# Kernel tuning notes

Measured on AMD Instinct MI355X. Metric: run time of the kernel, lower is better.

The kernel has to match this reference:

```python
import jax, jax.numpy as jnp
import numpy as np

NEG_SLOPE = 0.2


def _seg_sum(x, ids, n):
    return jax.ops.segment_sum(x, ids, num_segments=n)


def _seg_softmax(score, ids, n):
    # numerically stable segment softmax over segments `ids`
    m = jax.ops.segment_max(score, ids, num_segments=n)
    ex = jnp.exp(score - m[ids])
    denom = _seg_sum(ex, ids, n)
    return ex / denom[ids]


def _seg_mean(x, ids, n):
    s = _seg_sum(x, ids, n)
    cnt = _seg_sum(jnp.ones(ids.shape[0], x.dtype), ids, n)
    return jnp.where(cnt[:, None] > 0, s / jnp.maximum(cnt, 1.0)[:, None], 0.0)


def _dphgnn(X, V, E, S, Wx, bx, Wv, bv, a, Wt, bt, num_nodes, num_edges):
    X_init = X @ Wx + bx                         # [N, H]
    X_feat = X @ Wv + bv                         # [N, H]
    score_node = X_feat @ a                      # [N]
    score = jax.nn.leaky_relu(score_node[V], NEG_SLOPE)   # [nnz]
    w = _seg_softmax(score, E, num_edges)        # [nnz]
    Xev = X_feat[V] * w[:, None]                 # [nnz, H] gather + weight
    Y_v2e = jax.nn.elu(_seg_sum(Xev, E, num_edges))       # [M, H]
    e_msg = jnp.concatenate([Y_v2e, S], axis=1)  # [M, H+star]
    Y = e_msg @ Wt + bt                          # [M, H]
    Xn = _seg_mean(Y[E], V, num_nodes)           # [N, H]
    Xn = jax.nn.elu(Xn)                          # is_last=False, dropout=eval
    return Xn + X_init


def _hyperconv(X, V, E, Wf, bf, num_nodes, num_edges):
    Xn = X @ Wf + bf
    Y = _seg_mean(Xn[V], E, num_edges)           # [M, O]
    ones = jnp.ones(V.shape[0], jnp.float32)
    D_v = _seg_sum(ones, V, num_nodes)           # node degrees
    cnt_e = _seg_sum(ones, E, num_edges)
    # torch scatter_reduce(mean, include_self=True): zero init counts as one element
    De = _seg_sum(D_v[V], E, num_edges) / (cnt_e + 1.0)
    De_inv = jnp.where(De > 0, De ** -0.5, 1.0)
    Y = De_inv[:, None] * Y
    Xo = _seg_sum(Y[E], V, num_nodes)
    Dv_inv = jnp.where(D_v > 0, D_v ** -0.5, 0.0)
    return Dv_inv[:, None] * Xo                  # is_last=True: no relu/dropout


def setup_inputs() -> dict:
    key = jax.random.key(0)
    ks = jax.random.split(key, 24)
    N, M, NNZ = 50000, 20000, 400000
    IN, H, OUT, STAR = 128, 256, 128, 64

    def lin(k, i, o):
        s = 1.0 / np.sqrt(i)
        k1, k2 = jax.random.split(k)
        return (jax.random.uniform(k1, (i, o), jnp.float32, -s, s),
                jax.random.uniform(k2, (o,), jnp.float32, -s, s))

    X = jax.random.normal(ks[0], (N, IN), jnp.float32)
    V = jax.random.randint(ks[1], (NNZ,), 0, N).at[-1].set(N - 1)
    E = jax.random.randint(ks[2], (NNZ,), 0, M).at[-1].set(M - 1)
    S = jax.random.normal(ks[3], (M, STAR), jnp.float32)

    Wx0, bx0 = lin(ks[4], IN, H)
    Wv0, bv0 = lin(ks[5], IN, H)
    a0 = jax.random.uniform(ks[6], (H,), jnp.float32, -1/np.sqrt(H), 1/np.sqrt(H))
    Wt0, bt0 = lin(ks[7], H + STAR, H)
    Wx1, bx1 = lin(ks[8], H, H)
    Wv1, bv1 = lin(ks[9], H, H)
    a1 = jax.random.uniform(ks[10], (H,), jnp.float32, -1/np.sqrt(H), 1/np.sqrt(H))
    Wt1, bt1 = lin(ks[11], H + STAR, H)
    Wf, bf = lin(ks[12], H, OUT)

    return dict(X=X, V=V, E=E, S=S,
                Wx0=Wx0, bx0=bx0, Wv0=Wv0, bv0=bv0, a0=a0, Wt0=Wt0, bt0=bt0,
                Wx1=Wx1, bx1=bx1, Wv1=Wv1, bv1=bv1, a1=a1, Wt1=Wt1, bt1=bt1,
                Wf=Wf, bf=bf)


def reference(X, V, E, S, Wx0, bx0, Wv0, bv0, a0, Wt0, bt0,
              Wx1, bx1, Wv1, bv1, a1, Wt1, bt1, Wf, bf):
    N = X.shape[0]
    M = S.shape[0]
    h = _dphgnn(X, V, E, S, Wx0, bx0, Wv0, bv0, a0, Wt0, bt0, N, M)
    h = _dphgnn(h, V, E, S, Wx1, bx1, Wv1, bv1, a1, Wt1, bt1, N, M)
    out = _hyperconv(h, V, E, Wf, bf, N, M)
    return out
```

## Files before the change

### kernel.cpp

```cpp
#include <hip/hip_runtime.h>

typedef unsigned short u16;
typedef __attribute__((ext_vector_type(4))) u16 u16x4;
typedef __attribute__((ext_vector_type(8))) u16 u16x8;
typedef __attribute__((ext_vector_type(8))) _Float16 f16x8;
typedef __attribute__((ext_vector_type(4))) float f32x4;

__device__ __forceinline__ u16 f2h(float x) {
    _Float16 h = (_Float16)x;
    return __builtin_bit_cast(u16, h);
}
__device__ __forceinline__ float h2f(u16 u) {
    return (float)__builtin_bit_cast(_Float16, u);
}

__device__ __forceinline__ void gl_lds16(const void* g, void* l) {
    __builtin_amdgcn_global_load_lds(
        (const __attribute__((address_space(1))) void*)g,
        (__attribute__((address_space(3))) void*)l, 16, 0, 0);
}

__global__ __launch_bounds__(256) void gemm_mfma_kernel(
    const u16* __restrict__ A, int lda,
    const u16* __restrict__ B, int ldb,
    const float* __restrict__ biasF, const float* __restrict__ biasB,
    u16* __restrict__ CbA, u16* __restrict__ CbB,
    const float* __restrict__ avec, float* __restrict__ scoreOut,
    int M, int Nc, int ncSplit, int K, int nrb, int ncb)
{
    int g = blockIdx.x;
    int xcd = g & 7;
    int slot = g >> 3;
    int rbi = slot / ncb;
    int cb = slot - rbi * ncb;
    int rb = xcd + 8 * rbi;
    if (rb >= nrb) return;

    __shared__ __align__(16) u16 lds[12288];
    u16* sA0 = lds;
    u16* sA1 = lds + 4096;
    u16* sB0 = lds + 8192;
    u16* sB1 = lds + 10240;

    int tid = threadIdx.x;
    int wave = tid >> 6, lane = tid & 63;
    int row0 = rb * 128, col0 = cb * 64;

    long gA[2];
    int sOffA[2];
#pragma unroll
    for (int r = 0; r < 2; ++r) {
        int trow = r * 64 + wave * 16 + (lane >> 2);
        int chunk = (lane & 3) ^ ((trow >> 2) & 3);
        int arow = min(row0 + trow, M - 1);
        gA[r] = (long)arow * lda + chunk * 8;
        sOffA[r] = (r * 64 + wave * 16) * 32;
    }
    int trowB = wave * 16 + (lane >> 2);
    int chunkB = (lane & 3) ^ ((trowB >> 2) & 3);
    long gB = (long)(col0 + trowB) * ldb + chunkB * 8;
    int sOffB = (wave * 16) * 32;

    int m16 = lane & 15, quad = lane >> 4;
    int offA[4], offB[2];
#pragma unroll
    for (int i = 0; i < 4; ++i) {
        int ra = (wave & 1) * 64 + i * 16 + m16;
        offA[i] = ra * 32 + ((quad ^ ((ra >> 2) & 3)) * 8);
    }
#pragma unroll
    for (int j = 0; j < 2; ++j) {
        int rbx = (wave >> 1) * 32 + j * 16 + m16;
        offB[j] = rbx * 32 + ((quad ^ ((rbx >> 2) & 3)) * 8);
    }

    f32x4 acc[4][2];
#pragma unroll
    for (int i = 0; i < 4; ++i)
#pragma unroll
        for (int j = 0; j < 2; ++j) {
            f32x4 z = {0.f, 0.f, 0.f, 0.f};
            acc[i][j] = z;
        }

    int nkb = K >> 6;
    for (int kb = 0; kb < nkb; ++kb) {
#pragma unroll
        for (int r = 0; r < 2; ++r) {
            gl_lds16(A + gA[r], sA0 + sOffA[r]);
            gl_lds16(A + gA[r] + 32, sA1 + sOffA[r]);
        }
        gl_lds16(B + gB, sB0 + sOffB);
        gl_lds16(B + gB + 32, sB1 + sOffB);
        __syncthreads();
        {
            f16x8 av[4], bv[2];
#pragma unroll
            for (int i = 0; i < 4; ++i) av[i] = *(const f16x8*)(sA0 + offA[i]);
#pragma unroll
            for (int j = 0; j < 2; ++j) bv[j] = *(const f16x8*)(sB0 + offB[j]);
#pragma unroll
            for (int i = 0; i < 4; ++i)
#pragma unroll
                for (int j = 0; j < 2; ++j)
                    acc[i][j] = __builtin_amdgcn_mfma_f32_16x16x32_f16(av[i], bv[j], acc[i][j], 0, 0, 0);
        }
        {
            f16x8 av[4], bv[2];
#pragma unroll
            for (int i = 0; i < 4; ++i) av[i] = *(const f16x8*)(sA1 + offA[i]);
#pragma unroll
            for (int j = 0; j < 2; ++j) bv[j] = *(const f16x8*)(sB1 + offB[j]);
#pragma unroll
            for (int i = 0; i < 4; ++i)
#pragma unroll
                for (int j = 0; j < 2; ++j)
                    acc[i][j] = __builtin_amdgcn_mfma_f32_16x16x32_f16(av[i], bv[j], acc[i][j], 0, 0, 0);
        }
        __syncthreads();
#pragma unroll
        for (int r = 0; r < 2; ++r) gA[r] += 64;
        gB += 64;
    }

    int rbase = (wave & 1) * 64, cbase = (wave >> 1) * 32;
    float bj[2];
#pragma unroll
    for (int j = 0; j < 2; ++j) {
        int col = col0 + cbase + j * 16 + m16;
        bj[j] = (col >= ncSplit) ? biasB[col - ncSplit] : biasF[col];
    }
    u16* wlds = lds + wave * 2560;
    __syncthreads();
#pragma unroll
    for (int j = 0; j < 2; ++j)
#pragma unroll
        for (int i = 0; i < 4; ++i)
#pragma unroll
            for (int rr = 0; rr < 4; ++rr) {
                int lr = i * 16 + quad * 4 + rr;
                int lc = j * 16 + m16;
                int seg = (lc >> 3) ^ ((lr >> 2) & 3);
                wlds[lr * 40 + seg * 8 + (lc & 7)] = f2h(acc[i][j][rr] + bj[j]);
            }
    __syncthreads();
    {
        int colbase = col0 + cbase;
        bool isB = (colbase >= ncSplit);
        u16* Cp = isB ? CbB : CbA;
        int stride = isB ? (Nc - ncSplit) : ncSplit;
        int cc = isB ? (colbase - ncSplit) : colbase;
        bool doScore = (scoreOut != nullptr) && isB;
        int row = row0 + rbase + lane;
        if (row < M) {
            float sp = 0.f;
#pragma unroll
            for (int s = 0; s < 4; ++s) {
                int sseg = s ^ ((lane >> 2) & 3);
                u16x8 vv = *(const u16x8*)(wlds + lane * 40 + sseg * 8);
                *(u16x8*)(Cp + (size_t)row * stride + cc + s * 8) = vv;
                if (doScore) {
#pragma unroll
                    for (int q = 0; q < 8; ++q)
                        sp += h2f(vv[q]) * avec[cc + s * 8 + q];
                }
            }
            if (doScore) atomicAdd(scoreOut + row, sp);
        }
    }
}

struct WJob { const float* W; u16* Wt; int K; int ncShift; };
struct WJobs { WJob j[7]; };

__global__ void wsplit_all_kernel(WJobs jobs)
{
    WJob jb = jobs.j[blockIdx.y];
    int Nc = 1 << jb.ncShift;
    int idx = blockIdx.x * blockDim.x + threadIdx.x;
    if (idx >= jb.K * Nc) return;
    int k = idx >> jb.ncShift, n = idx & (Nc - 1);
    jb.Wt[(size_t)n * jb.K + k] = f2h(jb.W[idx]);
}

__global__ void cast_inputs_kernel(const float* __restrict__ X, u16* __restrict__ Abuf, int n4x,
                                   const float* __restrict__ S, u16* __restrict__ Ae, int nS)
{
    int id = blockIdx.x * blockDim.x + threadIdx.x;
    if (id < n4x) {
        float4 x = ((const float4*)X)[id];
        u16x4 h;
        h.x = f2h(x.x); h.y = f2h(x.y); h.z = f2h(x.z); h.w = f2h(x.w);
        *(u16x4*)(Abuf + (size_t)id * 4) = h;
    } else {
        int i = id - n4x;
        if (i < nS) {
            int e = i >> 6, c = i & 63;
            Ae[(size_t)e * 320 + 256 + c] = f2h(S[i]);
        }
    }
}

__global__ void count_kernel(const int* __restrict__ V, const int* __restrict__ E,
                             int* ecnt, int* ncnt, int nnz)
{
    int k = blockIdx.x * blockDim.x + threadIdx.x;
    if (k >= nnz) return;
    int e = E[k];
    int v = V[k];
    atomicAdd(&ecnt[e], 1);
    atomicAdd(&ncnt[v], 1);
}

__global__ void fill_kernel(const int* __restrict__ V, const int* __restrict__ E,
                            int* ecur, int* ncur, int* edge_v, int* node_e, int nnz)
{
    int k = blockIdx.x * blockDim.x + threadIdx.x;
    if (k >= nnz) return;
    int e = E[k];
    int v = V[k];
    int j = atomicAdd(&ecur[e], 1);
    int i = atomicAdd(&ncur[v], 1);
    edge_v[j] = v;
    node_e[i] = e;
}

__global__ __launch_bounds__(256) void scan_part1_dual(
    const int* __restrict__ cntE, int* __restrict__ offE, int* __restrict__ psumE, int nE, int nbE,
    const int* __restrict__ cntN, int* __restrict__ offN, int* __restrict__ psumN, int nN)
{
    const int* cnt; int* off; int* psum; int n; int b;
    if ((int)blockIdx.x < nbE) { cnt = cntE; off = offE; psum = psumE; n = nE; b = blockIdx.x; }
    else { cnt = cntN; off = offN; psum = psumN; n = nN; b = blockIdx.x - nbE; }

    __shared__ int tsum[256];
    int base = b * 1024;
    int t = threadIdx.x;
    int idx0 = base + t * 4;
    int4 c = make_int4(0, 0, 0, 0);
    if (idx0 + 3 < n) c = *(const int4*)(cnt + idx0);
    else {
        if (idx0 + 0 < n) c.x = cnt[idx0 + 0];
        if (idx0 + 1 < n) c.y = cnt[idx0 + 1];
        if (idx0 + 2 < n) c.z = cnt[idx0 + 2];
        if (idx0 + 3 < n) c.w = cnt[idx0 + 3];
    }
    int s = c.x + c.y + c.z + c.w;
    tsum[t] = s;
    __syncthreads();
    for (int o = 1; o < 256; o <<= 1) {
        int v = (t >= o) ? tsum[t - o] : 0;
        __syncthreads();
        tsum[t] += v;
        __syncthreads();
    }
    int run = tsum[t] - s;
    run += c.x; if (idx0 + 0 < n) off[idx0 + 1] = run;
    run += c.y; if (idx0 + 1 < n) off[idx0 + 2] = run;
    run += c.z; if (idx0 + 2 < n) off[idx0 + 3] = run;
    run += c.w; if (idx0 + 3 < n) off[idx0 + 4] = run;
    if (t == 255) psum[b] = tsum[255];
}

__global__ __launch_bounds__(256) void scan_part2_dual(
    const int* __restrict__ cntE, int* __restrict__ offE, const int* __restrict__ psumE,
    int* __restrict__ curE, int nE, int nbE,
    const int* __restrict__ cntN, int* __restrict__ offN, const int* __restrict__ psumN,
    int* __restrict__ curN, int nN)
{
    const int* cnt; int* off; const int* psum; int* cur; int n; int b;
    if ((int)blockIdx.x < nbE) { cnt = cntE; off = offE; psum = psumE; cur = curE; n = nE; b = blockIdx.x; }
    else { cnt = cntN; off = offN; psum = psumN; cur = curN; n = nN; b = blockIdx.x - nbE; }

    __shared__ int bpref;
    int t = threadIdx.x;
    if (t < 64) {
        int s = (t < b) ? psum[t] : 0;
#pragma unroll
        for (int o = 32; o; o >>= 1) s += __shfl_xor(s, o);
        if (t == 0) {
            bpref = s;
            if (b == 0) off[0] = 0;
        }
    }
    __syncthreads();
    int base = b * 1024 + t * 4;
#pragma unroll
    for (int q = 0; q < 4; ++q) {
        int i = base + q;
        if (i < n) {
            int inc = off[i + 1] + bpref;
            off[i + 1] = inc;
            cur[i] = inc - cnt[i];
        }
    }
}

__device__ __forceinline__ float lrelu(float s) { return s >= 0.f ? s : 0.2f * s; }

__global__ void v2e_fused_kernel(const u16* __restrict__ Xf,
                                 const float* __restrict__ score,
                                 const int* __restrict__ eoff,
                                 const int* __restrict__ edge_v,
                                 u16* __restrict__ Ae, int M)
{
    int e = blockIdx.x * 8 + (threadIdx.x >> 5);
    if (e >= M) return;
    int sl = threadIdx.x & 31;
    int j0 = eoff[e], j1 = eoff[e + 1];
    float m = -INFINITY;
    for (int j = j0 + sl; j < j1; j += 32) m = fmaxf(m, lrelu(score[edge_v[j]]));
#pragma unroll
    for (int o = 16; o; o >>= 1) m = fmaxf(m, __shfl_xor(m, o));
    float sum = 0.f;
    for (int j = j0 + sl; j < j1; j += 32) sum += expf(lrelu(score[edge_v[j]]) - m);
#pragma unroll
    for (int o = 16; o; o >>= 1) sum += __shfl_xor(sum, o);
    float inv = (j1 > j0) ? 1.0f / sum : 0.f;

    float acc[8] = {0.f, 0.f, 0.f, 0.f, 0.f, 0.f, 0.f, 0.f};
    int col = sl * 8;
    int j = j0;
    for (; j + 3 < j1; j += 4) {
        int v0 = edge_v[j + 0], v1 = edge_v[j + 1], v2 = edge_v[j + 2], v3 = edge_v[j + 3];
        float s0 = score[v0], s1 = score[v1], s2 = score[v2], s3 = score[v3];
        u16x8 r0 = *(const u16x8*)(Xf + (size_t)v0 * 256 + col);
        u16x8 r1 = *(const u16x8*)(Xf + (size_t)v1 * 256 + col);
        u16x8 r2 = *(const u16x8*)(Xf + (size_t)v2 * 256 + col);
        u16x8 r3 = *(const u16x8*)(Xf + (size_t)v3 * 256 + col);
        float w0 = expf(lrelu(s0) - m) * inv;
        float w1 = expf(lrelu(s1) - m) * inv;
        float w2 = expf(lrelu(s2) - m) * inv;
        float w3 = expf(lrelu(s3) - m) * inv;
#pragma unroll
        for (int q = 0; q < 8; ++q) {
            acc[q] += h2f(r0[q]) * w0;
            acc[q] += h2f(r1[q]) * w1;
            acc[q] += h2f(r2[q]) * w2;
            acc[q] += h2f(r3[q]) * w3;
        }
    }
    for (; j < j1; ++j) {
        int v = edge_v[j];
        float ww = expf(lrelu(score[v]) - m) * inv;
        u16x8 r = *(const u16x8*)(Xf + (size_t)v * 256 + col);
#pragma unroll
        for (int q = 0; q < 8; ++q) acc[q] += h2f(r[q]) * ww;
    }
    u16x8 hv;
#pragma unroll
    for (int q = 0; q < 8; ++q) {
        float vq = acc[q];
        vq = vq > 0.f ? vq : expm1f(vq);
        hv[q] = f2h(vq);
    }
    *(u16x8*)(Ae + (size_t)e * 320 + col) = hv;
}

__global__ void e2v_finish_kernel(const u16* __restrict__ Y,
                                  const int* __restrict__ noff,
                                  const int* __restrict__ node_e,
                                  const u16* __restrict__ Xinit,
                                  u16* __restrict__ H, int N)
{
    int v = blockIdx.x * 8 + (threadIdx.x >> 5);
    if (v >= N) return;
    int sl = threadIdx.x & 31;
    int col = sl * 8;
    int i0 = noff[v], i1 = noff[v + 1];
    float acc[8] = {0.f, 0.f, 0.f, 0.f, 0.f, 0.f, 0.f, 0.f};
    int i = i0;
    for (; i + 3 < i1; i += 4) {
        int e0 = node_e[i + 0], e1 = node_e[i + 1], e2 = node_e[i + 2], e3 = node_e[i + 3];
        u16x8 r0 = *(const u16x8*)(Y + (size_t)e0 * 256 + col);
        u16x8 r1 = *(const u16x8*)(Y + (size_t)e1 * 256 + col);
        u16x8 r2 = *(const u16x8*)(Y + (size_t)e2 * 256 + col);
        u16x8 r3 = *(const u16x8*)(Y + (size_t)e3 * 256 + col);
#pragma unroll
        for (int q = 0; q < 8; ++q) {
            acc[q] += h2f(r0[q]);
            acc[q] += h2f(r1[q]);
            acc[q] += h2f(r2[q]);
            acc[q] += h2f(r3[q]);
        }
    }
    for (; i < i1; ++i) {
        int e = node_e[i];
        u16x8 r = *(const u16x8*)(Y + (size_t)e * 256 + col);
#pragma unroll
        for (int q = 0; q < 8; ++q) acc[q] += h2f(r[q]);
    }
    float inv = (i1 > i0) ? 1.0f / (float)(i1 - i0) : 0.f;
    size_t base = (size_t)v * 256 + col;
    u16x8 xi = *(const u16x8*)(Xinit + base);
    u16x8 hv;
#pragma unroll
    for (int q = 0; q < 8; ++q) {
        float mm = acc[q] * inv;
        float oq = (mm > 0.f ? mm : expm1f(mm)) + h2f(xi[q]);
        hv[q] = f2h(oq);
    }
    *(u16x8*)(H + base) = hv;
}

__global__ void yh_kernel(const u16* __restrict__ Xc,
                          const int* __restrict__ eoff, const int* __restrict__ edge_v,
                          const int* __restrict__ noff, u16* __restrict__ Yh, int M)
{
    int e = blockIdx.x * 16 + (threadIdx.x >> 4);
    if (e >= M) return;
    int sl = threadIdx.x & 15;
    int col = sl * 8;
    int j0 = eoff[e], j1 = eoff[e + 1];

    float dsum = 0.f;
    for (int j = j0 + sl; j < j1; j += 16) {
        int v = edge_v[j];
        dsum += (float)(noff[v + 1] - noff[v]);
    }
#pragma unroll
    for (int o = 8; o; o >>= 1) dsum += __shfl_xor(dsum, o);
    float De = dsum / ((float)(j1 - j0) + 1.0f);
    float deinv = De > 0.f ? rsqrtf(De) : 1.0f;

    float acc[8] = {0.f, 0.f, 0.f, 0.f, 0.f, 0.f, 0.f, 0.f};
    int j = j0;
    for (; j + 3 < j1; j += 4) {
        int v0 = edge_v[j + 0], v1 = edge_v[j + 1], v2 = edge_v[j + 2], v3 = edge_v[j + 3];
        u16x8 r0 = *(const u16x8*)(Xc + (size_t)v0 * 128 + col);
        u16x8 r1 = *(const u16x8*)(Xc + (size_t)v1 * 128 + col);
        u16x8 r2 = *(const u16x8*)(Xc + (size_t)v2 * 128 + col);
        u16x8 r3 = *(const u16x8*)(Xc + (size_t)v3 * 128 + col);
#pragma unroll
        for (int q = 0; q < 8; ++q) {
            acc[q] += h2f(r0[q]);
            acc[q] += h2f(r1[q]);
            acc[q] += h2f(r2[q]);
            acc[q] += h2f(r3[q]);
        }
    }
    for (; j < j1; ++j) {
        int v = edge_v[j];
        u16x8 r = *(const u16x8*)(Xc + (size_t)v * 128 + col);
#pragma unroll
        for (int q = 0; q < 8; ++q) acc[q] += h2f(r[q]);
    }
    float sc = ((j1 > j0) ? 1.0f / (float)(j1 - j0) : 0.f) * deinv;
    u16x8 o8;
#pragma unroll
    for (int q = 0; q < 8; ++q) o8[q] = f2h(acc[q] * sc);
    *(u16x8*)(Yh + (size_t)e * 128 + col) = o8;
}

__global__ void xo_final_kernel(const u16* __restrict__ Yh,
                                const int* __restrict__ noff, const int* __restrict__ node_e,
                                float* __restrict__ out, int N)
{
    int v = blockIdx.x * 16 + (threadIdx.x >> 4);
    if (v >= N) return;
    int sl = threadIdx.x & 15;
    int col = sl * 8;
    int i0 = noff[v], i1 = noff[v + 1];
    float acc[8] = {0.f, 0.f, 0.f, 0.f, 0.f, 0.f, 0.f, 0.f};
    int i = i0;
    for (; i + 3 < i1; i += 4) {
        int e0 = node_e[i + 0], e1 = node_e[i + 1], e2 = node_e[i + 2], e3 = node_e[i + 3];
        u16x8 r0 = *(const u16x8*)(Yh + (size_t)e0 * 128 + col);
        u16x8 r1 = *(const u16x8*)(Yh + (size_t)e1 * 128 + col);
        u16x8 r2 = *(const u16x8*)(Yh + (size_t)e2 * 128 + col);
        u16x8 r3 = *(const u16x8*)(Yh + (size_t)e3 * 128 + col);
#pragma unroll
        for (int q = 0; q < 8; ++q) {
            acc[q] += h2f(r0[q]);
            acc[q] += h2f(r1[q]);
            acc[q] += h2f(r2[q]);
            acc[q] += h2f(r3[q]);
        }
    }
    for (; i < i1; ++i) {
        int e = node_e[i];
        u16x8 r = *(const u16x8*)(Yh + (size_t)e * 128 + col);
#pragma unroll
        for (int q = 0; q < 8; ++q) acc[q] += h2f(r[q]);
    }
    float sc = (i1 > i0) ? rsqrtf((float)(i1 - i0)) : 0.f;
    float4 oA, oB;
    oA.x = acc[0] * sc; oA.y = acc[1] * sc; oA.z = acc[2] * sc; oA.w = acc[3] * sc;
    oB.x = acc[4] * sc; oB.y = acc[5] * sc; oB.z = acc[6] * sc; oB.w = acc[7] * sc;
    float* d = out + (size_t)v * 128 + col;
    *(float4*)d = oA;
    *(float4*)(d + 4) = oB;
}

static void gemm(const u16* A, int lda,
                 const u16* B, int ldb,
                 const float* biasF, const float* biasB,
                 u16* CbA, u16* CbB,
                 const float* avec, float* scoreOut,
                 int M, int Nc, int ncSplit, int K,
                 hipStream_t stream)
{
    int nrb = (M + 127) / 128, ncb = Nc / 64;
    int nrb8 = ((nrb + 7) / 8) * 8;
    gemm_mfma_kernel<<<nrb8 * ncb, 256, 0, stream>>>(
        A, lda, B, ldb, biasF, biasB, CbA, CbB, avec, scoreOut, M, Nc, ncSplit, K, nrb, ncb);
}

static void run_layer(u16* A, int K,
                      const u16* WxvT,
                      const float* bx, const float* bv, const float* a,
                      const u16* WtT, const float* bt,
                      u16* Ae,
                      u16* XinitB, u16* Xfeatb, u16* Ybufb, float* score,
                      const int* eoff, const int* edge_v,
                      const int* noff, const int* node_e,
                      int N, int M, hipStream_t stream)
{
    gemm(A, K, WxvT, K, bx, bv, XinitB, Xfeatb, a, score, N, 512, 256, K, stream);
    v2e_fused_kernel<<<(M + 7) / 8, 256, 0, stream>>>(Xfeatb, score, eoff, edge_v, Ae, M);
    gemm(Ae, 320, WtT, 320, nullptr, bt, nullptr, Ybufb, nullptr, nullptr, M, 256, 0, 320, stream);
    e2v_finish_kernel<<<(N + 7) / 8, 256, 0, stream>>>(Ybufb, noff, node_e, XinitB, A, N);
}

extern "C" void kernel_launch(void* const* d_in, const int* in_sizes, int n_in,
                              void* d_out, int out_size, void* d_ws, size_t ws_size,
                              hipStream_t stream)
{
    const float* X   = (const float*)d_in[0];
    const int*   V   = (const int*)d_in[1];
    const int*   E   = (const int*)d_in[2];
    const float* S   = (const float*)d_in[3];
    const float* Wx0 = (const float*)d_in[4];  const float* bx0 = (const float*)d_in[5];
    const float* Wv0 = (const float*)d_in[6];  const float* bv0 = (const float*)d_in[7];
    const float* a0  = (const float*)d_in[8];
    const float* Wt0 = (const float*)d_in[9];  const float* bt0 = (const float*)d_in[10];
    const float* Wx1 = (const float*)d_in[11]; const float* bx1 = (const float*)d_in[12];
    const float* Wv1 = (const float*)d_in[13]; const float* bv1 = (const float*)d_in[14];
    const float* a1  = (const float*)d_in[15];
    const float* Wt1 = (const float*)d_in[16]; const float* bt1 = (const float*)d_in[17];
    const float* Wf  = (const float*)d_in[18]; const float* bf  = (const float*)d_in[19];

    int N   = in_sizes[0] / 128;
    int NNZ = in_sizes[1];
    int M   = in_sizes[3] / 64;

    float* ws = (float*)d_ws;
    size_t off = 0;
    u16* XinitB = (u16*)(ws + off); off += (size_t)N * 128;
    u16* XfeatR = (u16*)(ws + off); off += (size_t)N * 128;
    u16* Xfeatb = XfeatR;
    u16* Ybufb  = XfeatR;
    u16* Abuf = (u16*)(ws + off); off += (size_t)N * 128;
    u16* Ae   = (u16*)(ws + off); off += (size_t)M * 160;
    u16* WxvT0 = (u16*)(ws + off); off += (size_t)(512 * 128) / 2;
    u16* WtT0  = (u16*)(ws + off); off += (size_t)(256 * 320) / 2;
    u16* WxvT1 = (u16*)(ws + off); off += (size_t)(512 * 256) / 2;
    u16* WtT1  = (u16*)(ws + off); off += (size_t)(256 * 320) / 2;
    u16* WfT   = (u16*)(ws + off); off += (size_t)(128 * 256) / 2;
    int* ecnt   = (int*)(ws + off); off += (size_t)M;
    int* ncnt   = (int*)(ws + off); off += (size_t)N;
    float* score = ws + off;        off += (size_t)N;
    int* eoff   = (int*)(ws + off); off += (size_t)(M + 1);
    int* ecur   = (int*)(ws + off); off += (size_t)M;
    int* psumE  = (int*)(ws + off); off += 64;
    int* edge_v = (int*)(ws + off); off += (size_t)NNZ;
    int* noff   = (int*)(ws + off); off += (size_t)(N + 1);
    int* ncur   = (int*)(ws + off); off += (size_t)N;
    int* psumN  = (int*)(ws + off); off += 64;
    int* node_e = (int*)(ws + off); off += (size_t)NNZ;

    hipMemsetAsync(ecnt, 0, (size_t)(M + 2 * N) * 4, stream);
    count_kernel<<<(NNZ + 255) / 256, 256, 0, stream>>>(V, E, ecnt, ncnt, NNZ);
    int nbE = (M + 1023) / 1024, nbN = (N + 1023) / 1024;
    scan_part1_dual<<<nbE + nbN, 256, 0, stream>>>(ecnt, eoff, psumE, M, nbE,
                                                   ncnt, noff, psumN, N);
    scan_part2_dual<<<nbE + nbN, 256, 0, stream>>>(ecnt, eoff, psumE, ecur, M, nbE,
                                                   ncnt, noff, psumN, ncur, N);
    fill_kernel<<<(NNZ + 255) / 256, 256, 0, stream>>>(V, E, ecur, ncur, edge_v, node_e, NNZ);

    int n4x = N * 128 / 4, nS = M * 64;
    cast_inputs_kernel<<<(n4x + nS + 255) / 256, 256, 0, stream>>>(X, Abuf, n4x, S, Ae, nS);

    WJobs jobs;
    jobs.j[0] = {Wx0, WxvT0,             128, 8};
    jobs.j[1] = {Wv0, WxvT0 + 256 * 128, 128, 8};
    jobs.j[2] = {Wt0, WtT0,              320, 8};
    jobs.j[3] = {Wx1, WxvT1,             256, 8};
    jobs.j[4] = {Wv1, WxvT1 + 256 * 256, 256, 8};
    jobs.j[5] = {Wt1, WtT1,              320, 8};
    jobs.j[6] = {Wf,  WfT,               256, 7};
    dim3 wg((320 * 256 + 255) / 256, 7);
    wsplit_all_kernel<<<wg, 256, 0, stream>>>(jobs);

    run_layer(Abuf, 128, WxvT0, bx0, bv0, a0,
              WtT0, bt0, Ae, XinitB, Xfeatb, Ybufb, score,
              eoff, edge_v, noff, node_e, N, M, stream);
    hipMemsetAsync(score, 0, (size_t)N * 4, stream);
    run_layer(Abuf, 256, WxvT1, bx1, bv1, a1,
              WtT1, bt1, Ae, XinitB, Xfeatb, Ybufb, score,
              eoff, edge_v, noff, node_e, N, M, stream);

    u16* Xcb = XfeatR;
    u16* Yhb = XinitB;
    gemm(Abuf, 256, WfT, 256, bf, nullptr, Xcb, nullptr, nullptr, nullptr, N, 128, 128, 256, stream);
    yh_kernel<<<(M + 15) / 16, 256, 0, stream>>>(Xcb, eoff, edge_v, noff, Yhb, M);
    xo_final_kernel<<<(N + 15) / 16, 256, 0, stream>>>(Yhb, noff, node_e, (float*)d_out, N);
}
```

Baseline: 500.1 us.

## Fuse prep kernels and piggyback CSR fill onto GEMM launches

Merges the count, input-cast and weight-transpose kernels into a single block-partitioned prep kernel, with the count loop handling eight entries per thread. The CSR fill for edges is folded into extra blocks of the first GEMM and the node fill into the second GEMM, and the score memset is moved into extra blocks of the first e2v kernel. This removes several kernel launches and lets the atomic fill work overlap with GEMM blocks. In exchange the GEMM grid gets heterogeneous blocks and more parameters, and the fills now rely on stream ordering to finish before v2e and e2v consume edge_v and node_e.

```diff
diff --git a/kernel.cpp b/kernel.cpp
--- a/kernel.cpp
+++ b/kernel.cpp
@@ -26,9 +26,28 @@
     const float* __restrict__ biasF, const float* __restrict__ biasB,
     u16* __restrict__ CbA, u16* __restrict__ CbB,
     const float* __restrict__ avec, float* __restrict__ scoreOut,
+    const int* __restrict__ tKey, const int* __restrict__ tVal,
+    int* __restrict__ tCur, int* __restrict__ tOut, int tNnz, int tailBlocks,
     int M, int Nc, int ncSplit, int K, int nrb, int ncb)
 {
-    int g = blockIdx.x;
+    if ((int)blockIdx.x < tailBlocks) {
+        int k0 = ((int)blockIdx.x * 256 + (int)threadIdx.x) * 8;
+        if (k0 >= tNnz) return;
+        int kmax = min(tNnz - k0, 8);
+        int kk[8], vv[8], sl[8];
+        if (kmax == 8) {
+            int4 a = *(const int4*)(tKey + k0), b = *(const int4*)(tKey + k0 + 4);
+            int4 c = *(const int4*)(tVal + k0), d = *(const int4*)(tVal + k0 + 4);
+            kk[0]=a.x; kk[1]=a.y; kk[2]=a.z; kk[3]=a.w; kk[4]=b.x; kk[5]=b.y; kk[6]=b.z; kk[7]=b.w;
+            vv[0]=c.x; vv[1]=c.y; vv[2]=c.z; vv[3]=c.w; vv[4]=d.x; vv[5]=d.y; vv[6]=d.z; vv[7]=d.w;
+        } else {
+            for (int q = 0; q < kmax; ++q) { kk[q] = tKey[k0 + q]; vv[q] = tVal[k0 + q]; }
+        }
+        for (int q = 0; q < kmax; ++q) sl[q] = atomicAdd(&tCur[kk[q]], 1);
+        for (int q = 0; q < kmax; ++q) tOut[sl[q]] = vv[q];
+        return;
+    }
+    int g = (int)blockIdx.x - tailBlocks;
     int xcd = g & 7;
     int slot = g >> 3;
     int rbi = slot / ncb;
@@ -173,56 +192,55 @@
 struct WJob { const float* W; u16* Wt; int K; int ncShift; };
 struct WJobs { WJob j[7]; };
 
-__global__ void wsplit_all_kernel(WJobs jobs)
-{
-    WJob jb = jobs.j[blockIdx.y];
+__global__ void prep_fused_kernel(
+    const int* __restrict__ V, const int* __restrict__ E,
+    int* __restrict__ ecnt, int* __restrict__ ncnt, int nnz, int nbCnt,
+    const float* __restrict__ X, u16* __restrict__ Abuf, int n4x,
+    const float* __restrict__ S, u16* __restrict__ Ae, int nS, int nbCast,
+    WJobs jobs)
+{
+    int b = blockIdx.x;
+    if (b < nbCnt) {
+        int k0 = (b * 256 + (int)threadIdx.x) * 8;
+        if (k0 >= nnz) return;
+        int kmax = min(nnz - k0, 8);
+        int vv[8], ee[8];
+        if (kmax == 8) {
+            int4 a = *(const int4*)(V + k0), bb = *(const int4*)(V + k0 + 4);
+            int4 c = *(const int4*)(E + k0), d = *(const int4*)(E + k0 + 4);
+            vv[0]=a.x; vv[1]=a.y; vv[2]=a.z; vv[3]=a.w; vv[4]=bb.x; vv[5]=bb.y; vv[6]=bb.z; vv[7]=bb.w;
+            ee[0]=c.x; ee[1]=c.y; ee[2]=c.z; ee[3]=c.w; ee[4]=d.x; ee[5]=d.y; ee[6]=d.z; ee[7]=d.w;
+        } else {
+            for (int q = 0; q < kmax; ++q) { vv[q] = V[k0 + q]; ee[q] = E[k0 + q]; }
+        }
+        for (int q = 0; q < kmax; ++q) atomicAdd(&ecnt[ee[q]], 1);
+        for (int q = 0; q < kmax; ++q) atomicAdd(&ncnt[vv[q]], 1);
+        return;
+    }
+    if (b < nbCnt + nbCast) {
+        int id = (b - nbCnt) * 256 + (int)threadIdx.x;
+        if (id < n4x) {
+            float4 x = ((const float4*)X)[id];
+            u16x4 h;
+            h.x = f2h(x.x); h.y = f2h(x.y); h.z = f2h(x.z); h.w = f2h(x.w);
+            *(u16x4*)(Abuf + (size_t)id * 4) = h;
+        } else {
+            int i = id - n4x;
+            if (i < nS) {
+                int e = i >> 6, c = i & 63;
+                Ae[(size_t)e * 320 + 256 + c] = f2h(S[i]);
+            }
+        }
+        return;
+    }
+    int bb = b - nbCnt - nbCast;
+    int job = bb / 320, rem = bb - job * 320;
+    WJob jb = jobs.j[job];
     int Nc = 1 << jb.ncShift;
-    int idx = blockIdx.x * blockDim.x + threadIdx.x;
+    int idx = rem * 256 + (int)threadIdx.x;
     if (idx >= jb.K * Nc) return;
     int k = idx >> jb.ncShift, n = idx & (Nc - 1);
     jb.Wt[(size_t)n * jb.K + k] = f2h(jb.W[idx]);
-}
-
-__global__ void cast_inputs_kernel(const float* __restrict__ X, u16* __restrict__ Abuf, int n4x,
-                                   const float* __restrict__ S, u16* __restrict__ Ae, int nS)
-{
-    int id = blockIdx.x * blockDim.x + threadIdx.x;
-    if (id < n4x) {
-        float4 x = ((const float4*)X)[id];
-        u16x4 h;
-        h.x = f2h(x.x); h.y = f2h(x.y); h.z = f2h(x.z); h.w = f2h(x.w);
-        *(u16x4*)(Abuf + (size_t)id * 4) = h;
-    } else {
-        int i = id - n4x;
-        if (i < nS) {
-            int e = i >> 6, c = i & 63;
-            Ae[(size_t)e * 320 + 256 + c] = f2h(S[i]);
-        }
-    }
-}
-
-__global__ void count_kernel(const int* __restrict__ V, const int* __restrict__ E,
-                             int* ecnt, int* ncnt, int nnz)
-{
-    int k = blockIdx.x * blockDim.x + threadIdx.x;
-    if (k >= nnz) return;
-    int e = E[k];
-    int v = V[k];
-    atomicAdd(&ecnt[e], 1);
-    atomicAdd(&ncnt[v], 1);
-}
-
-__global__ void fill_kernel(const int* __restrict__ V, const int* __restrict__ E,
-                            int* ecur, int* ncur, int* edge_v, int* node_e, int nnz)
-{
-    int k = blockIdx.x * blockDim.x + threadIdx.x;
-    if (k >= nnz) return;
-    int e = E[k];
-    int v = V[k];
-    int j = atomicAdd(&ecur[e], 1);
-    int i = atomicAdd(&ncur[v], 1);
-    edge_v[j] = v;
-    node_e[i] = e;
 }
 
 __global__ __launch_bounds__(256) void scan_part1_dual(
@@ -361,9 +379,15 @@
                                   const int* __restrict__ noff,
                                   const int* __restrict__ node_e,
                                   const u16* __restrict__ Xinit,
-                                  u16* __restrict__ H, int N)
-{
-    int v = blockIdx.x * 8 + (threadIdx.x >> 5);
+                                  u16* __restrict__ H, int N,
+                                  float* __restrict__ zbuf, int zN, int zTail)
+{
+    if ((int)blockIdx.x < zTail) {
+        int id = (int)blockIdx.x * 256 + (int)threadIdx.x;
+        if (id < zN) zbuf[id] = 0.f;
+        return;
+    }
+    int v = ((int)blockIdx.x - zTail) * 8 + (threadIdx.x >> 5);
     if (v >= N) return;
     int sl = threadIdx.x & 31;
     int col = sl * 8;
@@ -497,29 +521,16 @@
                  const float* biasF, const float* biasB,
                  u16* CbA, u16* CbB,
                  const float* avec, float* scoreOut,
+                 const int* tKey, const int* tVal, int* tCur, int* tOut, int tNnz,
                  int M, int Nc, int ncSplit, int K,
                  hipStream_t stream)
 {
     int nrb = (M + 127) / 128, ncb = Nc / 64;
     int nrb8 = ((nrb + 7) / 8) * 8;
-    gemm_mfma_kernel<<<nrb8 * ncb, 256, 0, stream>>>(
-        A, lda, B, ldb, biasF, biasB, CbA, CbB, avec, scoreOut, M, Nc, ncSplit, K, nrb, ncb);
-}
-
-static void run_layer(u16* A, int K,
-                      const u16* WxvT,
-                      const float* bx, const float* bv, const float* a,
-                      const u16* WtT, const float* bt,
-                      u16* Ae,
-                      u16* XinitB, u16* Xfeatb, u16* Ybufb, float* score,
-                      const int* eoff, const int* edge_v,
-                      const int* noff, const int* node_e,
-                      int N, int M, hipStream_t stream)
-{
-    gemm(A, K, WxvT, K, bx, bv, XinitB, Xfeatb, a, score, N, 512, 256, K, stream);
-    v2e_fused_kernel<<<(M + 7) / 8, 256, 0, stream>>>(Xfeatb, score, eoff, edge_v, Ae, M);
-    gemm(Ae, 320, WtT, 320, nullptr, bt, nullptr, Ybufb, nullptr, nullptr, M, 256, 0, 320, stream);
-    e2v_finish_kernel<<<(N + 7) / 8, 256, 0, stream>>>(Ybufb, noff, node_e, XinitB, A, N);
+    int tailBlocks = (tKey != nullptr) ? (tNnz + 2047) / 2048 : 0;
+    gemm_mfma_kernel<<<nrb8 * ncb + tailBlocks, 256, 0, stream>>>(
+        A, lda, B, ldb, biasF, biasB, CbA, CbB, avec, scoreOut,
+        tKey, tVal, tCur, tOut, tNnz, tailBlocks, M, Nc, ncSplit, K, nrb, ncb);
 }
 
 extern "C" void kernel_launch(void* const* d_in, const int* in_sizes, int n_in,
@@ -570,17 +581,10 @@
     int* node_e = (int*)(ws + off); off += (size_t)NNZ;
 
     hipMemsetAsync(ecnt, 0, (size_t)(M + 2 * N) * 4, stream);
-    count_kernel<<<(NNZ + 255) / 256, 256, 0, stream>>>(V, E, ecnt, ncnt, NNZ);
-    int nbE = (M + 1023) / 1024, nbN = (N + 1023) / 1024;
-    scan_part1_dual<<<nbE + nbN, 256, 0, stream>>>(ecnt, eoff, psumE, M, nbE,
-                                                   ncnt, noff, psumN, N);
-    scan_part2_dual<<<nbE + nbN, 256, 0, stream>>>(ecnt, eoff, psumE, ecur, M, nbE,
-                                                   ncnt, noff, psumN, ncur, N);
-    fill_kernel<<<(NNZ + 255) / 256, 256, 0, stream>>>(V, E, ecur, ncur, edge_v, node_e, NNZ);
 
     int n4x = N * 128 / 4, nS = M * 64;
-    cast_inputs_kernel<<<(n4x + nS + 255) / 256, 256, 0, stream>>>(X, Abuf, n4x, S, Ae, nS);
-
+    int nbCnt = (NNZ + 2047) / 2048;
+    int nbCast = (n4x + nS + 255) / 256;
     WJobs jobs;
     jobs.j[0] = {Wx0, WxvT0,             128, 8};
     jobs.j[1] = {Wv0, WxvT0 + 256 * 128, 128, 8};
@@ -589,20 +593,39 @@
     jobs.j[4] = {Wv1, WxvT1 + 256 * 256, 256, 8};
     jobs.j[5] = {Wt1, WtT1,              320, 8};
     jobs.j[6] = {Wf,  WfT,               256, 7};
-    dim3 wg((320 * 256 + 255) / 256, 7);
-    wsplit_all_kernel<<<wg, 256, 0, stream>>>(jobs);
-
-    run_layer(Abuf, 128, WxvT0, bx0, bv0, a0,
-              WtT0, bt0, Ae, XinitB, Xfeatb, Ybufb, score,
-              eoff, edge_v, noff, node_e, N, M, stream);
-    hipMemsetAsync(score, 0, (size_t)N * 4, stream);
-    run_layer(Abuf, 256, WxvT1, bx1, bv1, a1,
-              WtT1, bt1, Ae, XinitB, Xfeatb, Ybufb, score,
-              eoff, edge_v, noff, node_e, N, M, stream);
+    int nbW = 7 * 320;
+    prep_fused_kernel<<<nbCnt + nbCast + nbW, 256, 0, stream>>>(
+        V, E, ecnt, ncnt, NNZ, nbCnt, X, Abuf, n4x, S, Ae, nS, nbCast, jobs);
+
+    int nbE = (M + 1023) / 1024, nbN = (N + 1023) / 1024;
+    scan_part1_dual<<<nbE + nbN, 256, 0, stream>>>(ecnt, eoff, psumE, M, nbE,
+                                                   ncnt, noff, psumN, N);
+    scan_part2_dual<<<nbE + nbN, 256, 0, stream>>>(ecnt, eoff, psumE, ecur, M, nbE,
+                                                   ncnt, noff, psumN, ncur, N);
+
+    gemm(Abuf, 128, WxvT0, 128, bx0, bv0, XinitB, Xfeatb, a0, score,
+         E, V, ecur, edge_v, NNZ, N, 512, 256, 128, stream);
+    v2e_fused_kernel<<<(M + 7) / 8, 256, 0, stream>>>(Xfeatb, score, eoff, edge_v, Ae, M);
+    gemm(Ae, 320, WtT0, 320, nullptr, bt0, nullptr, Ybufb, nullptr, nullptr,
+         V, E, ncur, node_e, NNZ, M, 256, 0, 320, stream);
+    {
+        int zTail = (N + 255) / 256;
+        e2v_finish_kernel<<<zTail + (N + 7) / 8, 256, 0, stream>>>(
+            Ybufb, noff, node_e, XinitB, Abuf, N, score, N, zTail);
+    }
+
+    gemm(Abuf, 256, WxvT1, 256, bx1, bv1, XinitB, Xfeatb, a1, score,
+         nullptr, nullptr, nullptr, nullptr, 0, N, 512, 256, 256, stream);
+    v2e_fused_kernel<<<(M + 7) / 8, 256, 0, stream>>>(Xfeatb, score, eoff, edge_v, Ae, M);
+    gemm(Ae, 320, WtT1, 320, nullptr, bt1, nullptr, Ybufb, nullptr, nullptr,
+         nullptr, nullptr, nullptr, nullptr, 0, M, 256, 0, 320, stream);
+    e2v_finish_kernel<<<(N + 7) / 8, 256, 0, stream>>>(
+        Ybufb, noff, node_e, XinitB, Abuf, N, nullptr, 0, 0);
 
     u16* Xcb = XfeatR;
     u16* Yhb = XinitB;
-    gemm(Abuf, 256, WfT, 256, bf, nullptr, Xcb, nullptr, nullptr, nullptr, N, 128, 128, 256, stream);
+    gemm(Abuf, 256, WfT, 256, bf, nullptr, Xcb, nullptr, nullptr, nullptr,
+         nullptr, nullptr, nullptr, nullptr, 0, N, 128, 128, 256, stream);
     yh_kernel<<<(M + 15) / 16, 256, 0, stream>>>(Xcb, eoff, edge_v, noff, Yhb, M);
     xo_final_kernel<<<(N + 15) / 16, 256, 0, stream>>>(Yhb, noff, node_e, (float*)d_out, N);
 }
```

Measured after the change: 467.6 us. 6.5% less time.
